# Kernel optimization log

Hardware: AMD Instinct MI355X
Metric: run time of the kernel (lower is better)

Reference implementation:

```python
import jax, jax.numpy as jnp
import numpy as np

N, E, H, FN, FE = 50000, 800000, 128, 8, 4


def setup_inputs() -> dict:
    key = jax.random.key(0)
    ks = jax.random.split(key, 12)
    g = lambda k, shape: jax.random.normal(k, shape, dtype=jnp.float32) * 0.05
    return dict(
        x=jax.random.normal(ks[0], (N, FN), dtype=jnp.float32),
        edge_index=jax.random.randint(ks[1], (2, E), 0, N),
        edge_attr=jax.random.normal(ks[2], (E, FE), dtype=jnp.float32),
        W1=g(ks[3], (FN, H)), b1=jnp.zeros((H,), jnp.float32),
        W2=g(ks[4], (H, H)), b2=jnp.zeros((H,), jnp.float32),
        W3=g(ks[5], (H, H)), b3=jnp.zeros((H,), jnp.float32),
        We1=g(ks[6], (FE, H)), be1=jnp.zeros((H,), jnp.float32),
        We2=g(ks[7], (H, H)), be2=jnp.zeros((H,), jnp.float32),
        Wc1=g(ks[8], (3 * H, H)), bc1=jnp.zeros((H,), jnp.float32),
        Wc2=g(ks[9], (H, H // 2)), bc2=jnp.zeros((H // 2,), jnp.float32),
        Wc3=g(ks[10], (H // 2, 2)), bc3=jnp.zeros((2,), jnp.float32),
    )


def _gcn(h, W, b, row2, col2, norm, n):
    # GCNConv: transform, normalized message from source row2 -> target col2, scatter-add, bias
    h = h @ W
    msg = norm[:, None] * h[row2]  # [E+N, H]
    return jax.ops.segment_sum(msg, col2, num_segments=n) + b


def reference(x, edge_index, edge_attr, W1, b1, W2, b2, W3, b3,
              We1, be1, We2, be2, Wc1, bc1, Wc2, bc2, Wc3, bc3):
    n = x.shape[0]
    row, col = edge_index[0], edge_index[1]
    loop = jnp.arange(n)
    # add self-loops (PyG GCNConv default)
    row2 = jnp.concatenate([row, loop])
    col2 = jnp.concatenate([col, loop])
    deg = jax.ops.segment_sum(jnp.ones_like(col2, dtype=x.dtype), col2, num_segments=n)
    dinv = jnp.where(deg > 0, deg ** -0.5, 0.0)
    norm = dinv[row2] * dinv[col2]  # symmetric normalization per edge

    h = jax.nn.relu(_gcn(x, W1, b1, row2, col2, norm, n))
    h = jax.nn.relu(_gcn(h, W2, b2, row2, col2, norm, n))
    h = jax.nn.relu(_gcn(h, W3, b3, row2, col2, norm, n))

    # edge encoder MLP (dropout inactive in eval)
    ef = jax.nn.relu(edge_attr @ We1 + be1) @ We2 + be2

    # gather endpoint node features, concat with edge features
    ec = jnp.concatenate([h[row], h[col], ef], axis=1)  # [E, 3H]
    z = jax.nn.relu(ec @ Wc1 + bc1)
    z = jax.nn.relu(z @ Wc2 + bc2)
    logits = z @ Wc3 + bc3
    return jax.nn.log_softmax(logits, axis=1)
```

## Files before the change

### kernel.cpp

```cpp
#include <hip/hip_runtime.h>
#include <math.h>

#define H 128
#define STC 152
#define SOT 136
#define SPQ 136
#define Z2S 69

typedef __attribute__((ext_vector_type(8))) short short8;
typedef __attribute__((ext_vector_type(4))) float f32x4;

__device__ inline float bflo(unsigned int v) { return __uint_as_float(v << 16); }
__device__ inline float bfhi(unsigned int v) { return __uint_as_float(v & 0xffff0000u); }
__device__ inline float bf2f(unsigned short v) { return __uint_as_float(((unsigned int)v) << 16); }

__device__ inline unsigned int cvtpk(float lo, float hi) {
    unsigned int r;
    asm("v_cvt_pk_bf16_f32 %0, %1, %2" : "=v"(r) : "v"(lo), "v"(hi));
    return r;
}
__device__ inline unsigned short f2bf1(float f) {
    unsigned int r;
    asm("v_cvt_pk_bf16_f32 %0, %1, %1" : "=v"(r) : "v"(f));
    return (unsigned short)r;
}

__device__ inline int permcol(int T, int lm) {
    return 32 * (T >> 1) + 2 * lm + (T & 1);
}
__device__ inline int kperm(int k) {
    int u = k >> 1;
    return 32 * (u >> 4) + (u & 15) + ((k & 1) << 4);
}


__global__ void count_kernel(const int* __restrict__ col, int E, int* __restrict__ cnt) {
    int e = blockIdx.x * blockDim.x + threadIdx.x;
    if (e < E) atomicAdd(&cnt[col[e]], 1);
}

__global__ void scan_sum_kernel(const int* __restrict__ cnt, int N, int* __restrict__ bsum) {
    int b = blockIdx.x, t = threadIdx.x;
    int base = b * 1024 + t * 4;
    int s = 0;
#pragma unroll
    for (int g = 0; g < 4; ++g) {
        int i = base + g;
        if (i < N) s += cnt[i];
    }
    for (int off = 32; off >= 1; off >>= 1) s += __shfl_down(s, off, 64);
    __shared__ int ws[4];
    if ((t & 63) == 0) ws[t >> 6] = s;
    __syncthreads();
    if (t == 0) bsum[b] = ws[0] + ws[1] + ws[2] + ws[3];
}

__global__ void scan_offsets_kernel(const int* __restrict__ bsum, int nb,
                                    int* __restrict__ boff, int* __restrict__ col_start, int N) {
    int lane = threadIdx.x;
    int v = (lane < nb) ? bsum[lane] : 0;
    int incl = v;
    for (int off = 1; off < 64; off <<= 1) {
        int u = __shfl_up(incl, off, 64);
        if (lane >= off) incl += u;
    }
    if (lane < nb) boff[lane] = incl - v;
    if (lane == 63) col_start[N] = incl;
}

__global__ void scan_write_kernel(const int* __restrict__ cnt, int N, const int* __restrict__ boff,
                                  int* __restrict__ col_start, int* __restrict__ cursor,
                                  float* __restrict__ dinv,
                                  const float* __restrict__ x, float* __restrict__ xs) {
    int b = blockIdx.x, t = threadIdx.x;
    int lane = t & 63, wv = t >> 6;
    int base = b * 1024 + t * 4;
    int c[4];
    int s = 0;
#pragma unroll
    for (int g = 0; g < 4; ++g) {
        int i = base + g;
        c[g] = (i < N) ? cnt[i] : 0;
        s += c[g];
    }
    int incl = s;
    for (int off = 1; off < 64; off <<= 1) {
        int u = __shfl_up(incl, off, 64);
        if (lane >= off) incl += u;
    }
    __shared__ int ws[4];
    if (lane == 63) ws[wv] = incl;
    __syncthreads();
    int run = boff[b] + incl - s;
    for (int w = 0; w < wv; ++w) run += ws[w];
#pragma unroll
    for (int g = 0; g < 4; ++g) {
        int i = base + g;
        if (i < N) {
            col_start[i] = run;
            cursor[i] = run;
            float di = rsqrtf((float)(c[g] + 1));
            dinv[i] = di;
            float4 xa = ((const float4*)x)[i * 2];
            float4 xb = ((const float4*)x)[i * 2 + 1];
            xa.x *= di; xa.y *= di; xa.z *= di; xa.w *= di;
            xb.x *= di; xb.y *= di; xb.z *= di; xb.w *= di;
            ((float4*)xs)[i * 2] = xa;
            ((float4*)xs)[i * 2 + 1] = xb;
            run += c[g];
        }
    }
}

__global__ void scatter_kernel(const int* __restrict__ row, const int* __restrict__ col, int E,
                               int* __restrict__ cursor, int* __restrict__ csc_src,
                               int2* __restrict__ csc_ec) {
    int e = blockIdx.x * blockDim.x + threadIdx.x;
    if (e < E) {
        int c = col[e];
        int p = atomicAdd(&cursor[c], 1);
        csc_src[p] = row[e];
        csc_ec[p] = make_int2(e, c);
    }
}


__global__ __launch_bounds__(256) void agg1x_kernel(
    const float* __restrict__ xs, const int* __restrict__ col_start,
    const int* __restrict__ csc_src, const float* __restrict__ dinv,
    const float* __restrict__ W, const float* __restrict__ b,
    unsigned int* __restrict__ out, int N) {
    int wv = threadIdx.x >> 6, lane = threadIdx.x & 63;
    int i = blockIdx.x * 4 + wv;
    if (i >= N) return;
    int f = lane & 7;
    int s0 = col_start[i], s1 = col_start[i + 1];
    float acc = 0.f;
    int p = s0 + (lane >> 3);
    for (; p + 8 < s1; p += 16) {
        int sa = csc_src[p], sb = csc_src[p + 8];
        acc += xs[sa * 8 + f] + xs[sb * 8 + f];
    }
    if (p < s1)
        acc += xs[csc_src[p] * 8 + f];
    acc += __shfl_xor(acc, 8, 64);
    acc += __shfl_xor(acc, 16, 64);
    acc += __shfl_xor(acc, 32, 64);
    float di = dinv[i];
    float av = di * (acc + xs[i * 8 + f]);
    float afv[8];
#pragma unroll
    for (int k = 0; k < 8; ++k) afv[k] = __shfl(av, k, 64);
    int j0 = 2 * lane;
    float a0 = b[j0], a1 = b[j0 + 1];
#pragma unroll
    for (int k = 0; k < 8; ++k) {
        a0 = fmaf(afv[k], W[k * 128 + j0], a0);
        a1 = fmaf(afv[k], W[k * 128 + j0 + 1], a1);
    }
    out[(size_t)i * 64 + lane] = cvtpk(di * fmaxf(a0, 0.f), di * fmaxf(a1, 0.f));
}

__global__ __launch_bounds__(256) void agg128bf_kernel(
    const unsigned int* __restrict__ hd, const int* __restrict__ col_start,
    const int* __restrict__ csc_src, const float* __restrict__ dinv,
    unsigned int* __restrict__ out, int N) {
    int wv = threadIdx.x >> 6, lane = threadIdx.x & 63;
    int i = blockIdx.x * 4 + wv;
    if (i >= N) return;
    int s0 = col_start[i], s1 = col_start[i + 1];
    float ax = 0.f, ay = 0.f;
    int p = s0;
    for (; p + 16 <= s1; p += 16) {
        unsigned int v[16];
#pragma unroll
        for (int k = 0; k < 16; ++k)
            v[k] = hd[(size_t)csc_src[p + k] * 64 + lane];
#pragma unroll
        for (int k = 0; k < 16; ++k) { ax += bflo(v[k]); ay += bfhi(v[k]); }
    }
    for (; p + 4 <= s1; p += 4) {
        unsigned int v0 = hd[(size_t)csc_src[p + 0] * 64 + lane];
        unsigned int v1 = hd[(size_t)csc_src[p + 1] * 64 + lane];
        unsigned int v2 = hd[(size_t)csc_src[p + 2] * 64 + lane];
        unsigned int v3 = hd[(size_t)csc_src[p + 3] * 64 + lane];
        ax += bflo(v0) + bflo(v1) + bflo(v2) + bflo(v3);
        ay += bfhi(v0) + bfhi(v1) + bfhi(v2) + bfhi(v3);
    }
    for (; p < s1; ++p) {
        unsigned int v = hd[(size_t)csc_src[p] * 64 + lane];
        ax += bflo(v); ay += bfhi(v);
    }
    float di = dinv[i];
    unsigned int vs = hd[(size_t)i * 64 + lane];
    float rx = di * (ax + bflo(vs));
    float ry = di * (ay + bfhi(vs));
    out[(size_t)i * 64 + lane] = cvtpk(rx, ry);
}

__global__ __launch_bounds__(256) void xform_mfma_kernel(
    const unsigned short* __restrict__ in, const unsigned short* __restrict__ Bp,
    const float* __restrict__ b, const float* __restrict__ scale,
    unsigned short* __restrict__ out, int N) {
    __shared__ __align__(16) unsigned short sm[64 * STC];
    int tid = threadIdx.x;
    int i0 = blockIdx.x * 64;
    for (int u = tid; u < 1024; u += 256) {
        int i = u >> 4, l = u & 15;
        int node = i0 + i; if (node >= N) node = N - 1;
        uint4 v = ((const uint4*)in)[(size_t)node * 16 + l];
        *(uint4*)&sm[i * STC + l * 8] = v;
    }
    __syncthreads();
    int lane = tid & 63, w = tid >> 6, lm = lane & 15, quad = lane >> 4;
    int nt0 = 2 * w, nt1 = 2 * w + 1;
    f32x4 acc0[4], acc1[4];
    {
        float bv0 = b[nt0 * 16 + lm], bv1 = b[nt1 * 16 + lm];
        for (int m = 0; m < 4; ++m)
            for (int r = 0; r < 4; ++r) { acc0[m][r] = bv0; acc1[m][r] = bv1; }
    }
#pragma unroll
    for (int s = 0; s < 4; ++s) {
        short8 b0 = *(const short8*)&Bp[((size_t)(s * 8 + nt0) * 64 + lane) * 8];
        short8 b1 = *(const short8*)&Bp[((size_t)(s * 8 + nt1) * 64 + lane) * 8];
#pragma unroll
        for (int m = 0; m < 4; ++m) {
            short8 afr = *(const short8*)&sm[(m * 16 + lm) * STC + s * 32 + quad * 8];
            acc0[m] = __builtin_amdgcn_mfma_f32_16x16x32_bf16(afr, b0, acc0[m], 0, 0, 0);
            acc1[m] = __builtin_amdgcn_mfma_f32_16x16x32_bf16(afr, b1, acc1[m], 0, 0, 0);
        }
    }
    __syncthreads();
    for (int m = 0; m < 4; ++m)
        for (int r = 0; r < 4; ++r) {
            int rw = m * 16 + quad * 4 + r;
            int node = i0 + rw; if (node >= N) node = N - 1;
            float sc = scale ? scale[node] : 1.f;
            sm[rw * SOT + nt0 * 16 + lm] = f2bf1(sc * fmaxf(acc0[m][r], 0.f));
            sm[rw * SOT + nt1 * 16 + lm] = f2bf1(sc * fmaxf(acc1[m][r], 0.f));
        }
    __syncthreads();
    for (int u = tid; u < 1024; u += 256) {
        int i = u >> 4, l = u & 15;
        int node = i0 + i;
        if (node < N)
            *(uint4*)&out[(size_t)node * 128 + l * 8] = *(uint4*)&sm[i * SOT + l * 8];
    }
}


__global__ void weff_kernel(const float* __restrict__ We2, const float* __restrict__ Wc1,
                            float* __restrict__ Weff) {
    int idx = blockIdx.x * blockDim.x + threadIdx.x;
    int k = idx >> 7, c = idx & 127;
    float acc = 0.f;
    for (int j = 0; j < 128; ++j)
        acc = fmaf(We2[k * 128 + j], Wc1[(256 + j) * 128 + c], acc);
    Weff[idx] = acc;
}

__global__ void prep_pack_kernel(
    const float* __restrict__ Wc1, const float* __restrict__ Weff,
    const float* __restrict__ W2, const float* __restrict__ W3,
    const float* __restrict__ Wc2, const float* __restrict__ We1,
    const float* __restrict__ be1, const float* __restrict__ bc1,
    const float* __restrict__ be2,
    unsigned short* __restrict__ BpA, unsigned short* __restrict__ BpB,
    unsigned short* __restrict__ BpU, unsigned short* __restrict__ BpW2,
    unsigned short* __restrict__ BpW3, unsigned short* __restrict__ Bp2,
    unsigned short* __restrict__ BpE, float* __restrict__ bc1p) {
    int b = blockIdx.x, tid = threadIdx.x;
    if (b < 40) {
        int which = b >> 3;
        const float* src = (which == 0) ? Wc1 : (which == 1) ? (Wc1 + 128 * 128)
                         : (which == 2) ? Weff : (which == 3) ? W2 : W3;
        unsigned short* dst = (which == 0) ? BpA : (which == 1) ? BpB
                            : (which == 2) ? BpU : (which == 3) ? BpW2 : BpW3;
        int idx = (b & 7) * 256 + tid;
        int s = idx >> 9, nt = (idx >> 6) & 7, lane = idx & 63;
        int quad = lane >> 4, lm = lane & 15;
        int n = nt * 16 + lm, k0 = s * 32 + quad * 8;
        unsigned int p[4];
#pragma unroll
        for (int g = 0; g < 4; ++g)
            p[g] = cvtpk(src[(k0 + 2 * g) * 128 + n], src[(k0 + 2 * g + 1) * 128 + n]);
        *(uint4*)&dst[(size_t)idx * 8] = make_uint4(p[0], p[1], p[2], p[3]);
    } else if (b < 44) {
        int idx = (b - 40) * 256 + tid;
        int s = idx >> 8, nt = (idx >> 6) & 3, lane = idx & 63;
        int quad = lane >> 4, lm = lane & 15;
        int n = nt * 16 + lm, k0 = s * 32 + quad * 8;
        unsigned int p[4];
#pragma unroll
        for (int g = 0; g < 4; ++g)
            p[g] = cvtpk(Wc2[kperm(k0 + 2 * g) * 64 + n], Wc2[kperm(k0 + 2 * g + 1) * 64 + n]);
        *(uint4*)&Bp2[(size_t)idx * 8] = make_uint4(p[0], p[1], p[2], p[3]);
    } else if (b < 46) {
        int idx = (b - 44) * 256 + tid;
        int nt = idx >> 6, lane = idx & 63;
        int quad = lane >> 4, lm = lane & 15;
        int n = nt * 16 + lm, k0 = quad * 8;
        unsigned int p[4];
#pragma unroll
        for (int g = 0; g < 4; ++g) {
            int r0 = k0 + 2 * g, r1 = r0 + 1;
            float v0 = (r0 < 4) ? We1[r0 * 128 + n] : ((r0 == 4) ? be1[n] : 0.f);
            float v1 = (r1 < 4) ? We1[r1 * 128 + n] : ((r1 == 4) ? be1[n] : 0.f);
            p[g] = cvtpk(v0, v1);
        }
        *(uint4*)&BpE[(size_t)idx * 8] = make_uint4(p[0], p[1], p[2], p[3]);
    } else {
        if (tid < 128) {
            float acc = bc1[tid];
            for (int j = 0; j < 128; ++j)
                acc = fmaf(be2[j], Wc1[(256 + j) * 128 + tid], acc);
            bc1p[tid] = acc;
        }
    }
}


__global__ __launch_bounds__(256) void h3pq_kernel(
    const unsigned short* __restrict__ in, const unsigned short* __restrict__ BpW3,
    const float* __restrict__ b3,
    const unsigned short* __restrict__ BpA, const unsigned short* __restrict__ BpB,
    const float* __restrict__ bc1p,
    unsigned short* __restrict__ P, unsigned short* __restrict__ Q, int N) {
    __shared__ __align__(16) unsigned short At[64 * STC];
    __shared__ __align__(16) unsigned short Hs[64 * SOT];
    int tid = threadIdx.x;
    int i0 = blockIdx.x * 64;
    for (int u = tid; u < 1024; u += 256) {
        int i = u >> 4, l = u & 15;
        int node = i0 + i; if (node >= N) node = N - 1;
        uint4 v = ((const uint4*)in)[(size_t)node * 16 + l];
        *(uint4*)&At[i * STC + l * 8] = v;
    }
    __syncthreads();
    int lane = tid & 63, w = tid >> 6, lm = lane & 15, quad = lane >> 4;

    {
        int nt0 = 2 * w, nt1 = 2 * w + 1;
        f32x4 a0[4], a1[4];
        float bv0 = b3[nt0 * 16 + lm], bv1 = b3[nt1 * 16 + lm];
        for (int m = 0; m < 4; ++m)
            for (int r = 0; r < 4; ++r) { a0[m][r] = bv0; a1[m][r] = bv1; }
#pragma unroll
        for (int s = 0; s < 4; ++s) {
            short8 b0 = *(const short8*)&BpW3[((size_t)(s * 8 + nt0) * 64 + lane) * 8];
            short8 b1 = *(const short8*)&BpW3[((size_t)(s * 8 + nt1) * 64 + lane) * 8];
#pragma unroll
            for (int m = 0; m < 4; ++m) {
                short8 afr = *(const short8*)&At[(m * 16 + lm) * STC + s * 32 + quad * 8];
                a0[m] = __builtin_amdgcn_mfma_f32_16x16x32_bf16(afr, b0, a0[m], 0, 0, 0);
                a1[m] = __builtin_amdgcn_mfma_f32_16x16x32_bf16(afr, b1, a1[m], 0, 0, 0);
            }
        }
        __syncthreads();
        for (int m = 0; m < 4; ++m)
            for (int r = 0; r < 4; ++r) {
                int rw = m * 16 + quad * 4 + r;
                Hs[rw * SOT + nt0 * 16 + lm] = f2bf1(fmaxf(a0[m][r], 0.f));
                Hs[rw * SOT + nt1 * 16 + lm] = f2bf1(fmaxf(a1[m][r], 0.f));
            }
    }
    __syncthreads();

    int half = w & 1;
    const unsigned short* Bp = (w >> 1) ? BpB : BpA;
    f32x4 acc[4][4];
    for (int nt = 0; nt < 4; ++nt) {
        float bv = (w >> 1) ? 0.f : bc1p[half * 64 + nt * 16 + lm];
        for (int m = 0; m < 4; ++m)
            for (int r = 0; r < 4; ++r) acc[nt][m][r] = bv;
    }
#pragma unroll
    for (int s = 0; s < 4; ++s) {
        short8 afr[4];
#pragma unroll
        for (int m = 0; m < 4; ++m)
            afr[m] = *(const short8*)&Hs[(m * 16 + lm) * SOT + s * 32 + quad * 8];
#pragma unroll
        for (int nt = 0; nt < 4; ++nt) {
            short8 bfr = *(const short8*)&Bp[((size_t)(s * 8 + half * 4 + nt) * 64 + lane) * 8];
#pragma unroll
            for (int m = 0; m < 4; ++m)
                acc[nt][m] = __builtin_amdgcn_mfma_f32_16x16x32_bf16(afr[m], bfr, acc[nt][m], 0, 0, 0);
        }
    }
    __syncthreads();

    {
        unsigned short* St = (w < 2) ? At : Hs;
        for (int nt = 0; nt < 4; ++nt) {
            int T = half * 4 + nt;
            int pc = permcol(T, lm);
            for (int m = 0; m < 4; ++m)
                for (int r = 0; r < 4; ++r) {
                    int rw = m * 16 + quad * 4 + r;
                    St[rw * SOT + pc] = f2bf1(acc[nt][m][r]);
                }
        }
    }
    __syncthreads();
    for (int u = tid; u < 1024; u += 256) {
        int i = u >> 4, l = u & 15;
        int node = i0 + i;
        if (node < N) {
            *(uint4*)&P[(size_t)node * 128 + l * 8] = *(uint4*)&At[i * SOT + l * 8];
            *(uint4*)&Q[(size_t)node * 128 + l * 8] = *(uint4*)&Hs[i * SOT + l * 8];
        }
    }
}


__global__ __launch_bounds__(256, 4) void classifier_mfma2(
    const int* __restrict__ csc_src, const int2* __restrict__ csc_ec,
    const float* __restrict__ ea, const unsigned short* __restrict__ BpE,
    const unsigned short* __restrict__ P, const unsigned short* __restrict__ Q,
    const unsigned short* __restrict__ BpU, const unsigned short* __restrict__ Bp2,
    const float* __restrict__ bc2, const float* __restrict__ Wc3, const float* __restrict__ bc3,
    float* __restrict__ out, int E) {
    __shared__ __align__(16) unsigned char smem[37888];
    unsigned short* SpqB = (unsigned short*)smem;
    float* z2 = (float*)smem;
    unsigned short* At = (unsigned short*)(smem + 17664);
    unsigned short* z1 = At;
    float* part = (float*)(smem + 17664);
    int* sS = (int*)(smem + 37120);
    int* eS = sS + 64;
    int* cS = eS + 64;

    int tid = threadIdx.x;
    int lane = tid & 63, w = tid >> 6, lm = lane & 15, quad = lane >> 4;
    int e0 = blockIdx.x * 64;

    short8 bE0 = *(const short8*)&BpE[((size_t)(2 * w) * 64 + lane) * 8];
    short8 bE1 = *(const short8*)&BpE[((size_t)(2 * w + 1) * 64 + lane) * 8];
    short8 b0s[4], b1s[4], b2s[4];
#pragma unroll
    for (int s = 0; s < 4; ++s) {
        b0s[s] = *(const short8*)&BpU[((size_t)(s * 8 + 2 * w) * 64 + lane) * 8];
        b1s[s] = *(const short8*)&BpU[((size_t)(s * 8 + 2 * w + 1) * 64 + lane) * 8];
        b2s[s] = *(const short8*)&Bp2[((size_t)(s * 4 + w) * 64 + lane) * 8];
    }
    float bv2 = bc2[w * 16 + lm];

    if (tid < 64) {
        int p = e0 + tid; if (p >= E) p = E - 1;
        sS[tid] = csc_src[p];
        int2 ec = csc_ec[p];
        eS[tid] = ec.x; cS[tid] = ec.y;
    }
    __syncthreads();

    float4 av[4];
    if (quad == 0) {
#pragma unroll
        for (int m = 0; m < 4; ++m)
            av[m] = ((const float4*)ea)[eS[m * 16 + lm]];
    }

    {
        const uint4* P4 = (const uint4*)P;
        const uint4* Q4 = (const uint4*)Q;
        int l = tid & 15;
        uint4 pv[4], qv[4];
#pragma unroll
        for (int j = 0; j < 4; ++j) {
            int i = (tid >> 4) + 16 * j;
            pv[j] = P4[(size_t)sS[i] * 16 + l];
            qv[j] = Q4[(size_t)cS[i] * 16 + l];
        }
#pragma unroll
        for (int j = 0; j < 4; ++j) {
            int i = (tid >> 4) + 16 * j;
            uint4 o;
            o.x = cvtpk(bflo(pv[j].x) + bflo(qv[j].x), bfhi(pv[j].x) + bfhi(qv[j].x));
            o.y = cvtpk(bflo(pv[j].y) + bflo(qv[j].y), bfhi(pv[j].y) + bfhi(qv[j].y));
            o.z = cvtpk(bflo(pv[j].z) + bflo(qv[j].z), bfhi(pv[j].z) + bfhi(qv[j].z));
            o.w = cvtpk(bflo(pv[j].w) + bflo(qv[j].w), bfhi(pv[j].w) + bfhi(qv[j].w));
            *(uint4*)&SpqB[i * SPQ + l * 8] = o;
        }
    }

    short8 eaf[4];
#pragma unroll
    for (int m = 0; m < 4; ++m) eaf[m] = (short8){0, 0, 0, 0, 0, 0, 0, 0};
    if (quad == 0) {
#pragma unroll
        for (int m = 0; m < 4; ++m) {
            eaf[m][0] = (short)f2bf1(av[m].x);
            eaf[m][1] = (short)f2bf1(av[m].y);
            eaf[m][2] = (short)f2bf1(av[m].z);
            eaf[m][3] = (short)f2bf1(av[m].w);
            eaf[m][4] = (short)0x3F80;
        }
    }

    {
        f32x4 zacc = {0.f, 0.f, 0.f, 0.f};
#pragma unroll
        for (int m = 0; m < 4; ++m) {
            f32x4 t0 = __builtin_amdgcn_mfma_f32_16x16x32_bf16(eaf[m], bE0, zacc, 0, 0, 0);
            f32x4 t1 = __builtin_amdgcn_mfma_f32_16x16x32_bf16(eaf[m], bE1, zacc, 0, 0, 0);
#pragma unroll
            for (int r = 0; r < 4; ++r) {
                int rw = m * 16 + quad * 4 + r;
                At[rw * STC + 32 * w + lm]      = f2bf1(fmaxf(t0[r], 0.f));
                At[rw * STC + 32 * w + 16 + lm] = f2bf1(fmaxf(t1[r], 0.f));
            }
        }
    }
    __syncthreads();

    f32x4 acc0[4], acc1[4];
    for (int m = 0; m < 4; ++m)
        for (int r = 0; r < 4; ++r) { acc0[m][r] = 0.f; acc1[m][r] = 0.f; }
#pragma unroll
    for (int s = 0; s < 4; ++s) {
#pragma unroll
        for (int m = 0; m < 4; ++m) {
            short8 afr = *(const short8*)&At[(m * 16 + lm) * STC + s * 32 + quad * 8];
            acc0[m] = __builtin_amdgcn_mfma_f32_16x16x32_bf16(afr, b0s[s], acc0[m], 0, 0, 0);
            acc1[m] = __builtin_amdgcn_mfma_f32_16x16x32_bf16(afr, b1s[s], acc1[m], 0, 0, 0);
        }
    }
    {
        const unsigned int* Spq32 = (const unsigned int*)SpqB;
        for (int m = 0; m < 4; ++m)
            for (int r = 0; r < 4; ++r) {
                int rw = m * 16 + quad * 4 + r;
                unsigned int pq = Spq32[rw * (SPQ / 2) + 16 * w + lm];
                acc0[m][r] = fmaxf(acc0[m][r] + bflo(pq), 0.f);
                acc1[m][r] = fmaxf(acc1[m][r] + bfhi(pq), 0.f);
            }
    }
    __syncthreads();
    {
        unsigned int* z1u = (unsigned int*)z1;
        for (int m = 0; m < 4; ++m)
            for (int r = 0; r < 4; ++r) {
                int rw = m * 16 + quad * 4 + r;
                z1u[rw * (STC / 2) + 16 * w + lm] = cvtpk(acc0[m][r], acc1[m][r]);
            }
    }
    __syncthreads();

    {
        f32x4 acc2[4];
        for (int m = 0; m < 4; ++m)
            for (int r = 0; r < 4; ++r) acc2[m][r] = bv2;
#pragma unroll
        for (int s = 0; s < 4; ++s) {
#pragma unroll
            for (int m = 0; m < 4; ++m) {
                short8 afr = *(const short8*)&z1[(m * 16 + lm) * STC + s * 32 + quad * 8];
                acc2[m] = __builtin_amdgcn_mfma_f32_16x16x32_bf16(afr, b2s[s], acc2[m], 0, 0, 0);
            }
        }
        for (int m = 0; m < 4; ++m)
            for (int r = 0; r < 4; ++r)
                z2[(m * 16 + quad * 4 + r) * Z2S + w * 16 + lm] = fmaxf(acc2[m][r], 0.f);
    }
    __syncthreads();

    {
        int e = tid & 63, q = tid >> 6;
        int c = q & 1, hf = q >> 1;
        const float* zr = z2 + e * Z2S + hf * 32;
        const float* wc = Wc3 + hf * 64 + c;
        float acc = 0.f;
#pragma unroll 8
        for (int kk = 0; kk < 32; ++kk)
            acc = fmaf(zr[kk], wc[2 * kk], acc);
        part[q * 64 + e] = acc;
    }
    __syncthreads();
    if (tid < 64) {
        int p = e0 + tid;
        if (p < E) {
            float l0 = bc3[0] + part[tid] + part[128 + tid];
            float l1 = bc3[1] + part[64 + tid] + part[192 + tid];
            float m = fmaxf(l0, l1);
            float lse = m + logf(expf(l0 - m) + expf(l1 - m));
            ((float2*)out)[eS[tid]] = make_float2(l0 - lse, l1 - lse);
        }
    }
}


extern "C" void kernel_launch(void* const* d_in, const int* in_sizes, int n_in,
                              void* d_out, int out_size, void* d_ws, size_t ws_size,
                              hipStream_t stream) {
    const float* x   = (const float*)d_in[0];
    const int*   ei  = (const int*)d_in[1];
    const float* ea  = (const float*)d_in[2];
    const float* W1  = (const float*)d_in[3];
    const float* b1  = (const float*)d_in[4];
    const float* W2  = (const float*)d_in[5];
    const float* b2  = (const float*)d_in[6];
    const float* W3  = (const float*)d_in[7];
    const float* b3  = (const float*)d_in[8];
    const float* We1 = (const float*)d_in[9];
    const float* be1 = (const float*)d_in[10];
    const float* We2 = (const float*)d_in[11];
    const float* be2 = (const float*)d_in[12];
    const float* Wc1 = (const float*)d_in[13];
    const float* bc1 = (const float*)d_in[14];
    const float* Wc2 = (const float*)d_in[15];
    const float* bc2 = (const float*)d_in[16];
    const float* Wc3 = (const float*)d_in[17];
    const float* bc3 = (const float*)d_in[18];
    float* out = (float*)d_out;

    int N = in_sizes[0] / 8;
    int E = in_sizes[1] / 2;
    const int* row = ei;
    const int* col = ei + E;
    int NB = (N + 1023) / 1024;
    int ntiles = (E + 63) / 64;

    char* w = (char*)d_ws;
    auto alloc = [&](size_t bytes) { void* p = (void*)w; w += (bytes + 255) & ~(size_t)255; return p; };
    int*   cnt       = (int*)alloc((size_t)N * 4);
    int*   col_start = (int*)alloc((size_t)(N + 1) * 4);
    int*   cursor    = (int*)alloc((size_t)N * 4);
    int*   csc_src   = (int*)alloc((size_t)E * 4);
    int2*  csc_ec    = (int2*)alloc((size_t)E * 8);
    float* dinv      = (float*)alloc((size_t)N * 4);
    int*   bsum      = (int*)alloc(64 * 4);
    int*   boff      = (int*)alloc(64 * 4);
    float* Weff      = (float*)alloc(128 * 128 * 4);
    float* bc1p      = (float*)alloc(128 * 4);
    unsigned short* BpA  = (unsigned short*)alloc(32768);
    unsigned short* BpB  = (unsigned short*)alloc(32768);
    unsigned short* BpU  = (unsigned short*)alloc(32768);
    unsigned short* BpW2 = (unsigned short*)alloc(32768);
    unsigned short* BpW3 = (unsigned short*)alloc(32768);
    unsigned short* Bp2  = (unsigned short*)alloc(16384);
    unsigned short* BpE  = (unsigned short*)alloc(8192);
    float* xs   = (float*)alloc((size_t)N * 8 * 4);
    unsigned short* bufA = (unsigned short*)alloc((size_t)N * H * 2);
    unsigned short* bufB = (unsigned short*)alloc((size_t)N * H * 2);
    unsigned short* Pm   = (unsigned short*)alloc((size_t)N * H * 2);
    unsigned short* Qm   = (unsigned short*)alloc((size_t)N * H * 2);

    hipMemsetAsync(cnt, 0, (size_t)N * 4, stream);
    count_kernel<<<(E + 255) / 256, 256, 0, stream>>>(col, E, cnt);
    scan_sum_kernel<<<NB, 256, 0, stream>>>(cnt, N, bsum);
    scan_offsets_kernel<<<1, 64, 0, stream>>>(bsum, NB, boff, col_start, N);
    scan_write_kernel<<<NB, 256, 0, stream>>>(cnt, N, boff, col_start, cursor, dinv, x, xs);
    scatter_kernel<<<(E + 255) / 256, 256, 0, stream>>>(row, col, E, cursor, csc_src, csc_ec);

    weff_kernel<<<64, 256, 0, stream>>>(We2, Wc1, Weff);
    prep_pack_kernel<<<47, 256, 0, stream>>>(Wc1, Weff, W2, W3, Wc2, We1, be1, bc1, be2,
                                             BpA, BpB, BpU, BpW2, BpW3, Bp2, BpE, bc1p);

    agg1x_kernel<<<(N + 3) / 4, 256, 0, stream>>>(xs, col_start, csc_src, dinv, W1, b1,
                                                  (unsigned int*)bufA, N);
    agg128bf_kernel<<<(N + 3) / 4, 256, 0, stream>>>((const unsigned int*)bufA, col_start, csc_src,
                                                     dinv, (unsigned int*)bufB, N);
    xform_mfma_kernel<<<(N + 63) / 64, 256, 0, stream>>>(bufB, BpW2, b2, dinv, bufA, N);
    agg128bf_kernel<<<(N + 3) / 4, 256, 0, stream>>>((const unsigned int*)bufA, col_start, csc_src,
                                                     dinv, (unsigned int*)bufB, N);
    h3pq_kernel<<<(N + 63) / 64, 256, 0, stream>>>(bufB, BpW3, b3, BpA, BpB, bc1p, Pm, Qm, N);

    classifier_mfma2<<<ntiles, 256, 0, stream>>>(
        csc_src, csc_ec, ea, BpE, Pm, Qm, BpU, Bp2, bc2, Wc3, bc3, out, E);
}
```

Before: 417.2 us.

## Gather P/Q directly into MFMA register layout and raise wave priority around MFMAs

The classifier kernel no longer stages the P+Q endpoint sums through shared memory. Each lane loads the 32-bit P and Q words it needs for its accumulator layout and adds them after the GEMM, which removes an LDS write/read pass. The trade is 32 narrow 4-byte gathers per thread instead of 16-byte coalesced ones, plus more registers held live across the MFMA loop. s_setprio(1/0) is also wrapped around the MFMA loops in several kernels so that math-phase waves get issue priority.

```diff
diff --git a/kernel.cpp b/kernel.cpp
--- a/kernel.cpp
+++ b/kernel.cpp
@@ -4,7 +4,6 @@
 #define H 128
 #define STC 152
 #define SOT 136
-#define SPQ 136
 #define Z2S 69
 
 typedef __attribute__((ext_vector_type(8))) short short8;
@@ -220,6 +219,7 @@
         for (int m = 0; m < 4; ++m)
             for (int r = 0; r < 4; ++r) { acc0[m][r] = bv0; acc1[m][r] = bv1; }
     }
+    __builtin_amdgcn_s_setprio(1);
 #pragma unroll
     for (int s = 0; s < 4; ++s) {
         short8 b0 = *(const short8*)&Bp[((size_t)(s * 8 + nt0) * 64 + lane) * 8];
@@ -231,6 +231,7 @@
             acc1[m] = __builtin_amdgcn_mfma_f32_16x16x32_bf16(afr, b1, acc1[m], 0, 0, 0);
         }
     }
+    __builtin_amdgcn_s_setprio(0);
     __syncthreads();
     for (int m = 0; m < 4; ++m)
         for (int r = 0; r < 4; ++r) {
@@ -346,6 +347,7 @@
         float bv0 = b3[nt0 * 16 + lm], bv1 = b3[nt1 * 16 + lm];
         for (int m = 0; m < 4; ++m)
             for (int r = 0; r < 4; ++r) { a0[m][r] = bv0; a1[m][r] = bv1; }
+        __builtin_amdgcn_s_setprio(1);
 #pragma unroll
         for (int s = 0; s < 4; ++s) {
             short8 b0 = *(const short8*)&BpW3[((size_t)(s * 8 + nt0) * 64 + lane) * 8];
@@ -357,6 +359,7 @@
                 a1[m] = __builtin_amdgcn_mfma_f32_16x16x32_bf16(afr, b1, a1[m], 0, 0, 0);
             }
         }
+        __builtin_amdgcn_s_setprio(0);
         __syncthreads();
         for (int m = 0; m < 4; ++m)
             for (int r = 0; r < 4; ++r) {
@@ -375,6 +378,7 @@
         for (int m = 0; m < 4; ++m)
             for (int r = 0; r < 4; ++r) acc[nt][m][r] = bv;
     }
+    __builtin_amdgcn_s_setprio(1);
 #pragma unroll
     for (int s = 0; s < 4; ++s) {
         short8 afr[4];
@@ -389,6 +393,7 @@
                 acc[nt][m] = __builtin_amdgcn_mfma_f32_16x16x32_bf16(afr[m], bfr, acc[nt][m], 0, 0, 0);
         }
     }
+    __builtin_amdgcn_s_setprio(0);
     __syncthreads();
 
     {
@@ -423,7 +428,6 @@
     const float* __restrict__ bc2, const float* __restrict__ Wc3, const float* __restrict__ bc3,
     float* __restrict__ out, int E) {
     __shared__ __align__(16) unsigned char smem[37888];
-    unsigned short* SpqB = (unsigned short*)smem;
     float* z2 = (float*)smem;
     unsigned short* At = (unsigned short*)(smem + 17664);
     unsigned short* z1 = At;
@@ -462,27 +466,19 @@
             av[m] = ((const float4*)ea)[eS[m * 16 + lm]];
     }
 
-    {
-        const uint4* P4 = (const uint4*)P;
-        const uint4* Q4 = (const uint4*)Q;
-        int l = tid & 15;
-        uint4 pv[4], qv[4];
-#pragma unroll
-        for (int j = 0; j < 4; ++j) {
-            int i = (tid >> 4) + 16 * j;
-            pv[j] = P4[(size_t)sS[i] * 16 + l];
-            qv[j] = Q4[(size_t)cS[i] * 16 + l];
-        }
-#pragma unroll
-        for (int j = 0; j < 4; ++j) {
-            int i = (tid >> 4) + 16 * j;
-            uint4 o;
-            o.x = cvtpk(bflo(pv[j].x) + bflo(qv[j].x), bfhi(pv[j].x) + bfhi(qv[j].x));
-            o.y = cvtpk(bflo(pv[j].y) + bflo(qv[j].y), bfhi(pv[j].y) + bfhi(qv[j].y));
-            o.z = cvtpk(bflo(pv[j].z) + bflo(qv[j].z), bfhi(pv[j].z) + bfhi(qv[j].z));
-            o.w = cvtpk(bflo(pv[j].w) + bflo(qv[j].w), bfhi(pv[j].w) + bfhi(qv[j].w));
-            *(uint4*)&SpqB[i * SPQ + l * 8] = o;
-        }
+    unsigned int pqp[4][4], pqq[4][4];
+    {
+        const unsigned int* P32 = (const unsigned int*)P;
+        const unsigned int* Q32 = (const unsigned int*)Q;
+        int cofs = 16 * w + lm;
+#pragma unroll
+        for (int m = 0; m < 4; ++m)
+#pragma unroll
+            for (int r = 0; r < 4; ++r) {
+                int rw = m * 16 + quad * 4 + r;
+                pqp[m][r] = P32[(size_t)sS[rw] * 64 + cofs];
+                pqq[m][r] = Q32[(size_t)cS[rw] * 64 + cofs];
+            }
     }
 
     short8 eaf[4];
@@ -501,6 +497,7 @@
 
     {
         f32x4 zacc = {0.f, 0.f, 0.f, 0.f};
+        __builtin_amdgcn_s_setprio(1);
 #pragma unroll
         for (int m = 0; m < 4; ++m) {
             f32x4 t0 = __builtin_amdgcn_mfma_f32_16x16x32_bf16(eaf[m], bE0, zacc, 0, 0, 0);
@@ -512,12 +509,14 @@
                 At[rw * STC + 32 * w + 16 + lm] = f2bf1(fmaxf(t1[r], 0.f));
             }
         }
+        __builtin_amdgcn_s_setprio(0);
     }
     __syncthreads();
 
     f32x4 acc0[4], acc1[4];
     for (int m = 0; m < 4; ++m)
         for (int r = 0; r < 4; ++r) { acc0[m][r] = 0.f; acc1[m][r] = 0.f; }
+    __builtin_amdgcn_s_setprio(1);
 #pragma unroll
     for (int s = 0; s < 4; ++s) {
 #pragma unroll
@@ -527,16 +526,14 @@
             acc1[m] = __builtin_amdgcn_mfma_f32_16x16x32_bf16(afr, b1s[s], acc1[m], 0, 0, 0);
         }
     }
-    {
-        const unsigned int* Spq32 = (const unsigned int*)SpqB;
-        for (int m = 0; m < 4; ++m)
-            for (int r = 0; r < 4; ++r) {
-                int rw = m * 16 + quad * 4 + r;
-                unsigned int pq = Spq32[rw * (SPQ / 2) + 16 * w + lm];
-                acc0[m][r] = fmaxf(acc0[m][r] + bflo(pq), 0.f);
-                acc1[m][r] = fmaxf(acc1[m][r] + bfhi(pq), 0.f);
-            }
-    }
+    __builtin_amdgcn_s_setprio(0);
+#pragma unroll
+    for (int m = 0; m < 4; ++m)
+#pragma unroll
+        for (int r = 0; r < 4; ++r) {
+            acc0[m][r] = fmaxf(acc0[m][r] + bflo(pqp[m][r]) + bflo(pqq[m][r]), 0.f);
+            acc1[m][r] = fmaxf(acc1[m][r] + bfhi(pqp[m][r]) + bfhi(pqq[m][r]), 0.f);
+        }
     __syncthreads();
     {
         unsigned int* z1u = (unsigned int*)z1;
@@ -552,6 +549,7 @@
         f32x4 acc2[4];
         for (int m = 0; m < 4; ++m)
             for (int r = 0; r < 4; ++r) acc2[m][r] = bv2;
+        __builtin_amdgcn_s_setprio(1);
 #pragma unroll
         for (int s = 0; s < 4; ++s) {
 #pragma unroll
@@ -560,6 +558,7 @@
                 acc2[m] = __builtin_amdgcn_mfma_f32_16x16x32_bf16(afr, b2s[s], acc2[m], 0, 0, 0);
             }
         }
+        __builtin_amdgcn_s_setprio(0);
         for (int m = 0; m < 4; ++m)
             for (int r = 0; r < 4; ++r)
                 z2[(m * 16 + quad * 4 + r) * Z2S + w * 16 + lm] = fmaxf(acc2[m][r], 0.f);
```

After: 425.2 us. Within noise of the previous version (+1.9%).
